# Optimization experiments

Hardware: AMD Instinct MI355X
Metric: run time of the kernel (lower is better)

## Reference

```python
import jax, jax.numpy as jnp
import numpy as np

NEG_SLOPE = 0.2  # PyG GATConv default negative_slope
EPS = 1e-16     # PyG softmax denominator epsilon


def gat_layer(x, src, dst, W, att_src, att_dst, bias, N):
    """PyG-style GATConv: gather -> leaky-relu score -> segment softmax -> scatter-add.
    x: [N, F_in], W: [F_in, H*C], att_src/att_dst: [H, C], bias: [H*C].
    src/dst: [E] edge endpoints (messages flow src -> dst), self-loops included.
    """
    H, C = att_src.shape
    h = (x @ W).reshape(N, H, C)                       # [N, H, C]
    a_s = jnp.sum(h * att_src, axis=-1)                # [N, H]
    a_d = jnp.sum(h * att_dst, axis=-1)                # [N, H]
    e = a_s[src] + a_d[dst]                            # [E, H]
    e = jnp.where(e > 0, e, NEG_SLOPE * e)             # leaky relu
    m = jax.ops.segment_max(e, dst, num_segments=N)    # [N, H] (self-loops ensure every node hit)
    p = jnp.exp(e - m[dst])                            # [E, H]
    s = jax.ops.segment_sum(p, dst, num_segments=N)    # [N, H]
    alpha = p / (s[dst] + EPS)                         # [E, H]
    out = jax.ops.segment_sum(alpha[:, :, None] * h[src], dst, num_segments=N)  # [N, H, C]
    return out.reshape(N, H * C) + bias


def setup_inputs() -> dict:
    key = jax.random.key(0)
    ks = jax.random.split(key, 12)
    N, E = 100000, 1600000
    x = jax.random.normal(ks[0], (N, 1), dtype=jnp.float32)
    edge_index = jax.random.randint(ks[1], (2, E), 0, N, dtype=jnp.int32)
    sc = 0.1
    # conv1: in=1, heads=4, out=8
    W1 = jax.random.normal(ks[2], (1, 32), dtype=jnp.float32) * sc
    att_src1 = jax.random.normal(ks[3], (4, 8), dtype=jnp.float32) * sc
    att_dst1 = jax.random.normal(ks[4], (4, 8), dtype=jnp.float32) * sc
    bias1 = jnp.zeros((32,), dtype=jnp.float32)
    # conv2: in=32, heads=8, out=8
    W2 = jax.random.normal(ks[5], (32, 64), dtype=jnp.float32) * sc
    att_src2 = jax.random.normal(ks[6], (8, 8), dtype=jnp.float32) * sc
    att_dst2 = jax.random.normal(ks[7], (8, 8), dtype=jnp.float32) * sc
    bias2 = jnp.zeros((64,), dtype=jnp.float32)
    # fc2: 64 -> 1
    fc_w = jax.random.normal(ks[8], (64, 1), dtype=jnp.float32) * sc
    fc_b = jnp.zeros((1,), dtype=jnp.float32)
    return {"x": x, "edge_index": edge_index,
            "W1": W1, "att_src1": att_src1, "att_dst1": att_dst1, "bias1": bias1,
            "W2": W2, "att_src2": att_src2, "att_dst2": att_dst2, "bias2": bias2,
            "fc_w": fc_w, "fc_b": fc_b}


def reference(x, edge_index, W1, att_src1, att_dst1, bias1,
              W2, att_src2, att_dst2, bias2, fc_w, fc_b):
    N = x.shape[0]
    loop = jnp.arange(N, dtype=edge_index.dtype)       # add_self_loops=True (PyG default)
    src = jnp.concatenate([edge_index[0], loop])
    dst = jnp.concatenate([edge_index[1], loop])
    h = jax.nn.elu(gat_layer(x, src, dst, W1, att_src1, att_dst1, bias1, N))
    h = jax.nn.elu(gat_layer(h, src, dst, W2, att_src2, att_dst2, bias2, N))
    return h @ fc_w + fc_b                             # [N, 1]
```

## Files before the change

kernel.cpp:

```cpp
#include <hip/hip_runtime.h>
#include <hip/hip_fp16.h>
#include <cmath>

#define TPB 256
#define NSLOPE 0.2f
#define SEPS 1e-16f

#define BSH 7
#define BNODES 128
#define NBMAX 1024
#define NCHUNK 512
#define SCTPB 1024
#define SCSTAGE 3360
#define STAGE 2816
#define MAXDEG 96

__device__ __forceinline__ float lrelu(float v) { return v > 0.f ? v : NSLOPE * v; }
__device__ __forceinline__ float elu1(float v)  { return v > 0.f ? v : expm1f(v); }
__device__ __forceinline__ float elu1f(float v) { return v > 0.f ? v : __expf(v) - 1.f; }

__global__ void k_prep(const float* __restrict__ W1, const float* __restrict__ as1,
                       const float* __restrict__ ad1, float* __restrict__ SD,
                       unsigned* __restrict__ bucketCursor, int NB, unsigned cap) {
    int t = threadIdx.x;
    for (int i = t; i < NB; i += blockDim.x) bucketCursor[(size_t)i * 16] = (unsigned)i * cap;
    if (t < 8) {
        int h = t & 3;
        const float* att = (t >= 4) ? ad1 : as1;
        float acc = 0.f;
        #pragma unroll
        for (int c = 0; c < 8; ++c) acc += W1[h*8+c] * att[h*8+c];
        SD[t] = acc;
    }
}

__global__ void k_bscatter(const int* __restrict__ srcI, const int* __restrict__ dstI,
                           int E, int N, int NB, int chunk,
                           unsigned* __restrict__ bucketCursor, int* __restrict__ pk) {
    __shared__ int cnt[NBMAX];
    __shared__ unsigned base[NBMAX];
    __shared__ int offl[NBMAX];
    __shared__ int rval[SCSTAGE];
    __shared__ unsigned short rbkt[SCSTAGE];
    int t = threadIdx.x;
    int ET = E + N;
    int beg = blockIdx.x * chunk;
    int end = min(beg + chunk, ET);
    int m = end - beg;
    for (int i = t; i < NBMAX; i += blockDim.x) cnt[i] = 0;
    __syncthreads();
    for (int e = beg + t; e < end; e += blockDim.x) {
        int d = (e < E) ? dstI[e] : (e - E);
        atomicAdd(&cnt[d >> BSH], 1);
    }
    __syncthreads();
    int v = (t < NBMAX) ? cnt[t] : 0;
    if (t < NBMAX) base[t] = (unsigned)v;
    __syncthreads();
    for (int off = 1; off < NBMAX; off <<= 1) {
        unsigned u = (t >= off && t < NBMAX) ? base[t - off] : 0u;
        __syncthreads();
        if (t < NBMAX) base[t] += u;
        __syncthreads();
    }
    if (t < NBMAX) offl[t] = (int)base[t] - v;
    __syncthreads();
    if (t < NB) {
        base[t] = v ? atomicAdd(&bucketCursor[(size_t)t * 16], (unsigned)v) : 0u;
        cnt[t] = 0;
    }
    __syncthreads();
    if (m <= SCSTAGE) {
        for (int e = beg + t; e < end; e += blockDim.x) {
            int s, d;
            if (e < E) { s = srcI[e]; d = dstI[e]; } else { s = d = e - E; }
            int b = d >> BSH;
            int r = atomicAdd(&cnt[b], 1);
            int slot = offl[b] + r;
            rval[slot] = (s << BSH) | (d & (BNODES - 1));
            rbkt[slot] = (unsigned short)b;
        }
        __syncthreads();
        for (int slot = t; slot < m; slot += blockDim.x) {
            int b = rbkt[slot];
            pk[base[b] + (unsigned)(slot - offl[b])] = rval[slot];
        }
    } else {
        for (int e = beg + t; e < end; e += blockDim.x) {
            int s, d;
            if (e < E) { s = srcI[e]; d = dstI[e]; } else { s = d = e - E; }
            int b = d >> BSH;
            int r = atomicAdd(&cnt[b], 1);
            pk[base[b] + (unsigned)r] = (s << BSH) | (d & (BNODES - 1));
        }
    }
}

__global__ void k_sl1h2(const int* __restrict__ pk, const unsigned* __restrict__ bucketCursor,
                        unsigned cap,
                        const float* __restrict__ x, const float* __restrict__ SD,
                        const float* __restrict__ W1, const float* __restrict__ b1,
                        const float* __restrict__ W2, const float* __restrict__ attS,
                        const float* __restrict__ attD, int N,
                        unsigned* __restrict__ offsets, int* __restrict__ sortedSrc,
                        __half* __restrict__ h2h, float* __restrict__ aS, float* __restrict__ aD) {
    __shared__ int sorted[STAGE];
    __shared__ int cnt[BNODES];
    __shared__ int offl[BNODES];
    __shared__ float lds1[BNODES][36];
    int b = blockIdx.x, t = threadIdx.x;
    unsigned rbeg = (unsigned)b * cap;
    int m = (int)(bucketCursor[(size_t)b * 16] - rbeg);
    bool inLds = (m <= STAGE);
    int base = b << BSH;
    if (t < BNODES) cnt[t] = 0;
    __syncthreads();
    for (int i = t; i < m; i += TPB) atomicAdd(&cnt[pk[rbeg + i] & (BNODES - 1)], 1);
    __syncthreads();
    int v = (t < BNODES) ? cnt[t] : 0;
    if (t < BNODES) offl[t] = v;
    __syncthreads();
    for (int off = 1; off < BNODES; off <<= 1) {
        int u = (t >= off && t < BNODES) ? offl[t - off] : 0;
        __syncthreads();
        if (t < BNODES) offl[t] += u;
        __syncthreads();
    }
    if (t < BNODES) {
        int ex = offl[t] - v;
        int d = base + t;
        if (d < N) offsets[d] = ((rbeg + (unsigned)ex) << 10) | (unsigned)v;
        cnt[t] = 0;
        offl[t] = ex;
    }
    __syncthreads();
    if (inLds) {
        for (int i = t; i < m; i += TPB) {
            int p = pk[rbeg + i];
            int dl = p & (BNODES - 1);
            int r = atomicAdd(&cnt[dl], 1);
            sorted[offl[dl] + r] = p >> BSH;
        }
        __syncthreads();
        for (int i = t; i < m; i += TPB) sortedSrc[rbeg + i] = sorted[i];
    } else {
        for (int i = t; i < m; i += TPB) {
            int p = pk[rbeg + i];
            int dl = p & (BNODES - 1);
            int r = atomicAdd(&cnt[dl], 1);
            sortedSrc[rbeg + (unsigned)(offl[dl] + r)] = p >> BSH;
        }
        __syncthreads();
    }
    __syncthreads();
    int n = t >> 1, half = t & 1;
    int d2 = base + n;
    bool active = (d2 < N);
    float s0 = 0.f, s1 = 0.f, s2 = 0.f, s3 = 0.f;
    float g0 = 0.f, g1 = 0.f, g2 = 0.f, g3 = 0.f;
    if (active) {
        int deg = cnt[n];
        int lbeg = offl[n];
        float xd = x[d2];
        float S0 = SD[0], S1 = SD[1], S2 = SD[2], S3 = SD[3];
        float D0 = xd*SD[4], D1 = xd*SD[5], D2 = xd*SD[6], D3 = xd*SD[7];
        int dh = (deg + 1) >> 1;
        int i = lbeg + (half ? dh : 0);
        int rem = half ? (deg - dh) : dh;
        for (; rem >= 2; rem -= 2, i += 2) {
            int a0 = inLds ? sorted[i]   : sortedSrc[rbeg + i];
            int a1 = inLds ? sorted[i+1] : sortedSrc[rbeg + i + 1];
            float x0 = x[a0], x1 = x[a1];
            float p;
            p = __expf(lrelu(x0*S0 + D0)); s0 += p; g0 += p * x0;
            p = __expf(lrelu(x0*S1 + D1)); s1 += p; g1 += p * x0;
            p = __expf(lrelu(x0*S2 + D2)); s2 += p; g2 += p * x0;
            p = __expf(lrelu(x0*S3 + D3)); s3 += p; g3 += p * x0;
            p = __expf(lrelu(x1*S0 + D0)); s0 += p; g0 += p * x1;
            p = __expf(lrelu(x1*S1 + D1)); s1 += p; g1 += p * x1;
            p = __expf(lrelu(x1*S2 + D2)); s2 += p; g2 += p * x1;
            p = __expf(lrelu(x1*S3 + D3)); s3 += p; g3 += p * x1;
        }
        if (rem > 0) {
            int a0 = inLds ? sorted[i] : sortedSrc[rbeg + i];
            float xs = x[a0];
            float p;
            p = __expf(lrelu(xs*S0 + D0)); s0 += p; g0 += p * xs;
            p = __expf(lrelu(xs*S1 + D1)); s1 += p; g1 += p * xs;
            p = __expf(lrelu(xs*S2 + D2)); s2 += p; g2 += p * xs;
            p = __expf(lrelu(xs*S3 + D3)); s3 += p; g3 += p * xs;
        }
    }
    s0 += __shfl_xor(s0, 1); s1 += __shfl_xor(s1, 1);
    s2 += __shfl_xor(s2, 1); s3 += __shfl_xor(s3, 1);
    g0 += __shfl_xor(g0, 1); g1 += __shfl_xor(g1, 1);
    g2 += __shfl_xor(g2, 1); g3 += __shfl_xor(g3, 1);
    if (active) {
        float gg[4];
        gg[0] = g0 / (s0 + SEPS); gg[1] = g1 / (s1 + SEPS);
        gg[2] = g2 / (s2 + SEPS); gg[3] = g3 / (s3 + SEPS);
        int h0 = half * 2;
        #pragma unroll
        for (int hh = 0; hh < 2; ++hh)
            #pragma unroll
            for (int cc = 0; cc < 8; ++cc)
                lds1[n][(h0+hh)*8+cc] = elu1(gg[h0+hh] * W1[(h0+hh)*8+cc] + b1[(h0+hh)*8+cc]);
    }
    __syncthreads();
    int lane = t & 63;
    int sub = t >> 6;
    float w2r[32];
    #pragma unroll
    for (int k = 0; k < 32; ++k) w2r[k] = W2[k*64 + lane];
    float attSl = attS[lane], attDl = attD[lane];
    int nCnt = min(BNODES, N - base);
    for (int nn = sub; nn < nCnt; nn += 4) {
        const float4* row4 = (const float4*)lds1[nn];
        float acc = 0.f;
        #pragma unroll
        for (int k4 = 0; k4 < 8; ++k4) {
            float4 rv = row4[k4];
            acc += rv.x*w2r[4*k4] + rv.y*w2r[4*k4+1] + rv.z*w2r[4*k4+2] + rv.w*w2r[4*k4+3];
        }
        int node = base + nn;
        h2h[(size_t)node*64 + lane] = __float2half(acc);
        float ps = acc * attSl;
        float pd = acc * attDl;
        #pragma unroll
        for (int mm = 1; mm < 8; mm <<= 1) {
            ps += __shfl_xor(ps, mm);
            pd += __shfl_xor(pd, mm);
        }
        int hh = lane >> 3, cc = lane & 7;
        if (cc == 0) aS[(size_t)node*8 + hh] = ps;
        if (cc == 1) aD[(size_t)node*8 + hh] = pd;
    }
}

__global__ void k_agg(const unsigned* __restrict__ offsets, const int* __restrict__ ss,
                      const float* __restrict__ aS, const float* __restrict__ aD,
                      const __half* __restrict__ h2h, const float* __restrict__ b2,
                      const float* __restrict__ fcw, const float* __restrict__ fcb,
                      float* __restrict__ out, int N) {
    __shared__ float pl[4][MAXDEG * 8];
    __shared__ int   sl[4][MAXDEG];
    int lane = threadIdx.x & 63;
    int w = threadIdx.x >> 6;
    int d = blockIdx.x * 4 + w;
    if (d >= N) return;
    unsigned u = offsets[d];
    unsigned beg = u >> 10;
    int deg = (int)(u & 1023u);
    int lH   = lane & 31;
    int half = lane >> 5;
    int hh   = lH >> 2;
    float sum = 0.f, ax = 0.f, ay = 0.f;
    if (deg <= MAXDEG) {
        for (int j = lane; j < deg; j += 64) sl[w][j] = ss[beg + j];
        float adp = aD[(size_t)d*8 + (lane & 7)];
        int tot = deg * 8;
        for (int base = 0; base < tot; base += 64) {
            int idx = base + lane;
            if (idx < tot) {
                int s = sl[w][idx >> 3];
                pl[w][idx] = __expf(lrelu(aS[(size_t)s*8 + (lane & 7)] + adp));
            }
        }
        int e = 0;
        for (; e + 8 <= deg; e += 8) {
            int e0 = e + half, e1 = e + 2 + half, e2 = e + 4 + half, e3 = e + 6 + half;
            int s0 = sl[w][e0], s1 = sl[w][e1], s2 = sl[w][e2], s3 = sl[w][e3];
            float p0 = pl[w][e0*8 + hh], p1 = pl[w][e1*8 + hh];
            float p2 = pl[w][e2*8 + hh], p3 = pl[w][e3*8 + hh];
            float2 g0 = __half22float2(*(const __half2*)(h2h + (size_t)s0*64 + 2*lH));
            float2 g1 = __half22float2(*(const __half2*)(h2h + (size_t)s1*64 + 2*lH));
            float2 g2 = __half22float2(*(const __half2*)(h2h + (size_t)s2*64 + 2*lH));
            float2 g3 = __half22float2(*(const __half2*)(h2h + (size_t)s3*64 + 2*lH));
            ax += p0*g0.x + p1*g1.x + p2*g2.x + p3*g3.x;
            ay += p0*g0.y + p1*g1.y + p2*g2.y + p3*g3.y;
            sum += (p0 + p1) + (p2 + p3);
        }
        for (; e + 2 <= deg; e += 2) {
            int e0 = e + half;
            int s0 = sl[w][e0];
            float p0 = pl[w][e0*8 + hh];
            float2 g0 = __half22float2(*(const __half2*)(h2h + (size_t)s0*64 + 2*lH));
            ax += p0*g0.x; ay += p0*g0.y; sum += p0;
        }
        if (e < deg) {
            int s0 = sl[w][e];
            float p0 = (half == 0) ? pl[w][e*8 + hh] : 0.f;
            float2 g0 = __half22float2(*(const __half2*)(h2h + (size_t)s0*64 + 2*lH));
            ax += p0*g0.x; ay += p0*g0.y; sum += p0;
        }
    } else {
        float adh = aD[(size_t)d*8 + hh];
        for (int e = half; e < deg; e += 2) {
            int s = ss[beg + e];
            float p = __expf(lrelu(aS[(size_t)s*8 + hh] + adh));
            float2 g = __half22float2(*(const __half2*)(h2h + (size_t)s*64 + 2*lH));
            ax += p*g.x; ay += p*g.y; sum += p;
        }
    }
    ax  += __shfl_xor(ax, 32);
    ay  += __shfl_xor(ay, 32);
    sum += __shfl_xor(sum, 32);
    float inv = 1.f / (sum + SEPS);
    float tt = elu1f(ax*inv + b2[2*lH]) * fcw[2*lH]
             + elu1f(ay*inv + b2[2*lH+1]) * fcw[2*lH+1];
    #pragma unroll
    for (int m = 16; m; m >>= 1) tt += __shfl_xor(tt, m);
    if (lane == 0) out[d] = tt + fcb[0];
}

extern "C" void kernel_launch(void* const* d_in, const int* in_sizes, int n_in,
                              void* d_out, int out_size, void* d_ws, size_t ws_size,
                              hipStream_t stream) {
    const float* x    = (const float*)d_in[0];
    const int*   ei   = (const int*)  d_in[1];
    const float* W1   = (const float*)d_in[2];
    const float* as1  = (const float*)d_in[3];
    const float* ad1  = (const float*)d_in[4];
    const float* b1   = (const float*)d_in[5];
    const float* W2   = (const float*)d_in[6];
    const float* attS2= (const float*)d_in[7];
    const float* attD2= (const float*)d_in[8];
    const float* b2   = (const float*)d_in[9];
    const float* fcw  = (const float*)d_in[10];
    const float* fcb  = (const float*)d_in[11];
    float* out = (float*)d_out;

    int N = in_sizes[0];
    int E = in_sizes[1] / 2;
    int ET = E + N;
    int NB = (N + BNODES - 1) / BNODES;
    unsigned cap = (unsigned)((ET + NB - 1) / NB + 512);
    cap = (cap + 3u) & ~3u;
    size_t padded = (size_t)NB * cap;

    const int* srcI = ei;
    const int* dstI = ei + E;

    float* ws = (float*)d_ws;
    size_t off = 0;
    float*    SD           = ws + off; off += 16;
    unsigned* bucketCursor = (unsigned*)(ws + off); off += (size_t)NBMAX * 16;
    unsigned* offsets      = (unsigned*)(ws + off); off += (size_t)N + 16;
    int*      pk           = (int*)(ws + off); off += padded;
    int*      sortedSrc    = (int*)(ws + off); off += padded;
    float*    aS2          = ws + off; off += (size_t)N * 8;
    float*    aD2          = ws + off; off += (size_t)N * 8;
    __half*   h2h          = (__half*)(ws + off); off += (size_t)N * 32;

    k_prep<<<1, 1024, 0, stream>>>(W1, as1, ad1, SD, bucketCursor, NB, cap);

    int chunk = (ET + NCHUNK - 1) / NCHUNK;
    k_bscatter<<<NCHUNK, SCTPB, 0, stream>>>(srcI, dstI, E, N, NB, chunk, bucketCursor, pk);
    k_sl1h2   <<<NB, TPB, 0, stream>>>(pk, bucketCursor, cap, x, SD, W1, b1, W2, attS2, attD2,
                                       N, offsets, sortedSrc, h2h, aS2, aD2);
    k_agg     <<<(N + 3) / 4, TPB, 0, stream>>>(offsets, sortedSrc, aS2, aD2, h2h,
                                                b2, fcw, fcb, out, N);
}
```

Measured before the change: 215.5 us.

## Split layer-2 aggregation into two head-group passes over half-width feature tables

The fp16 layer-2 feature table is stored as two separate planes, each holding 4 heads (32 channels) per node. Aggregation then runs in two kernel launches, one per plane, and the second accumulates into the output. Each pass gathers from a table half the size, which is meant to improve cache hit rates for the random source gathers. In exchange the edge list, attention scores and softmax sums are read and computed twice, and there is an extra launch.

```diff
diff --git a/kernel.cpp b/kernel.cpp
--- a/kernel.cpp
+++ b/kernel.cpp
@@ -103,7 +103,7 @@
                         const float* __restrict__ W2, const float* __restrict__ attS,
                         const float* __restrict__ attD, int N,
                         unsigned* __restrict__ offsets, int* __restrict__ sortedSrc,
-                        __half* __restrict__ h2h, float* __restrict__ aS, float* __restrict__ aD) {
+                        __half* __restrict__ h2p, float* __restrict__ aS, float* __restrict__ aD) {
     __shared__ int sorted[STAGE];
     __shared__ int cnt[BNODES];
     __shared__ int offl[BNODES];
@@ -213,6 +213,9 @@
     #pragma unroll
     for (int k = 0; k < 32; ++k) w2r[k] = W2[k*64 + lane];
     float attSl = attS[lane], attDl = attD[lane];
+    size_t N32 = (size_t)N * 32;
+    size_t tabOff = (size_t)(lane >> 5) * N32;
+    int ch = lane & 31;
     int nCnt = min(BNODES, N - base);
     for (int nn = sub; nn < nCnt; nn += 4) {
         const float4* row4 = (const float4*)lds1[nn];
@@ -223,7 +226,7 @@
             acc += rv.x*w2r[4*k4] + rv.y*w2r[4*k4+1] + rv.z*w2r[4*k4+2] + rv.w*w2r[4*k4+3];
         }
         int node = base + nn;
-        h2h[(size_t)node*64 + lane] = __float2half(acc);
+        h2p[tabOff + (size_t)node*32 + ch] = __float2half(acc);
         float ps = acc * attSl;
         float pd = acc * attDl;
         #pragma unroll
@@ -237,12 +240,12 @@
     }
 }
 
-__global__ void k_agg(const unsigned* __restrict__ offsets, const int* __restrict__ ss,
-                      const float* __restrict__ aS, const float* __restrict__ aD,
-                      const __half* __restrict__ h2h, const float* __restrict__ b2,
-                      const float* __restrict__ fcw, const float* __restrict__ fcb,
-                      float* __restrict__ out, int N) {
-    __shared__ float pl[4][MAXDEG * 8];
+__global__ void k_aggp(const unsigned* __restrict__ offsets, const int* __restrict__ ss,
+                       const float* __restrict__ aS, const float* __restrict__ aD,
+                       const __half* __restrict__ h2p, const float* __restrict__ b2,
+                       const float* __restrict__ fcw, const float* __restrict__ fcb,
+                       float* __restrict__ out, int N, int pass) {
+    __shared__ float pl[4][MAXDEG * 4];
     __shared__ int   sl[4][MAXDEG];
     int lane = threadIdx.x & 63;
     int w = threadIdx.x >> 6;
@@ -251,66 +254,64 @@
     unsigned u = offsets[d];
     unsigned beg = u >> 10;
     int deg = (int)(u & 1023u);
-    int lH   = lane & 31;
-    int half = lane >> 5;
-    int hh   = lH >> 2;
+    int eS = lane >> 4;
+    int pr = lane & 15;
+    int hL = pr >> 2;
+    int ho = pass * 4;
+    const __half* tab = h2p + (size_t)pass * ((size_t)N * 32);
     float sum = 0.f, ax = 0.f, ay = 0.f;
     if (deg <= MAXDEG) {
         for (int j = lane; j < deg; j += 64) sl[w][j] = ss[beg + j];
-        float adp = aD[(size_t)d*8 + (lane & 7)];
-        int tot = deg * 8;
+        float adp = aD[(size_t)d*8 + ho + (lane & 3)];
+        int tot = deg * 4;
         for (int base = 0; base < tot; base += 64) {
             int idx = base + lane;
             if (idx < tot) {
-                int s = sl[w][idx >> 3];
-                pl[w][idx] = __expf(lrelu(aS[(size_t)s*8 + (lane & 7)] + adp));
+                int s = sl[w][idx >> 2];
+                pl[w][idx] = __expf(lrelu(aS[(size_t)s*8 + ho + (lane & 3)] + adp));
             }
         }
         int e = 0;
         for (; e + 8 <= deg; e += 8) {
-            int e0 = e + half, e1 = e + 2 + half, e2 = e + 4 + half, e3 = e + 6 + half;
-            int s0 = sl[w][e0], s1 = sl[w][e1], s2 = sl[w][e2], s3 = sl[w][e3];
-            float p0 = pl[w][e0*8 + hh], p1 = pl[w][e1*8 + hh];
-            float p2 = pl[w][e2*8 + hh], p3 = pl[w][e3*8 + hh];
-            float2 g0 = __half22float2(*(const __half2*)(h2h + (size_t)s0*64 + 2*lH));
-            float2 g1 = __half22float2(*(const __half2*)(h2h + (size_t)s1*64 + 2*lH));
-            float2 g2 = __half22float2(*(const __half2*)(h2h + (size_t)s2*64 + 2*lH));
-            float2 g3 = __half22float2(*(const __half2*)(h2h + (size_t)s3*64 + 2*lH));
-            ax += p0*g0.x + p1*g1.x + p2*g2.x + p3*g3.x;
-            ay += p0*g0.y + p1*g1.y + p2*g2.y + p3*g3.y;
-            sum += (p0 + p1) + (p2 + p3);
-        }
-        for (; e + 2 <= deg; e += 2) {
-            int e0 = e + half;
-            int s0 = sl[w][e0];
-            float p0 = pl[w][e0*8 + hh];
-            float2 g0 = __half22float2(*(const __half2*)(h2h + (size_t)s0*64 + 2*lH));
-            ax += p0*g0.x; ay += p0*g0.y; sum += p0;
-        }
-        if (e < deg) {
-            int s0 = sl[w][e];
-            float p0 = (half == 0) ? pl[w][e*8 + hh] : 0.f;
-            float2 g0 = __half22float2(*(const __half2*)(h2h + (size_t)s0*64 + 2*lH));
-            ax += p0*g0.x; ay += p0*g0.y; sum += p0;
+            int ea = e + eS, eb = e + 4 + eS;
+            int sa = sl[w][ea], sb = sl[w][eb];
+            float pa = pl[w][ea*4 + hL], pb = pl[w][eb*4 + hL];
+            float2 ga = __half22float2(*(const __half2*)(tab + (size_t)sa*32 + 2*pr));
+            float2 gb = __half22float2(*(const __half2*)(tab + (size_t)sb*32 + 2*pr));
+            ax += pa*ga.x + pb*gb.x;
+            ay += pa*ga.y + pb*gb.y;
+            sum += pa + pb;
+        }
+        for (; e < deg; e += 4) {
+            int ea = e + eS;
+            bool ok = ea < deg;
+            int sa = sl[w][ok ? ea : 0];
+            float pa = ok ? pl[w][ea*4 + hL] : 0.f;
+            float2 ga = __half22float2(*(const __half2*)(tab + (size_t)sa*32 + 2*pr));
+            ax += pa*ga.x; ay += pa*ga.y; sum += pa;
         }
     } else {
-        float adh = aD[(size_t)d*8 + hh];
-        for (int e = half; e < deg; e += 2) {
+        float adh = aD[(size_t)d*8 + ho + hL];
+        for (int e = eS; e < deg; e += 4) {
             int s = ss[beg + e];
-            float p = __expf(lrelu(aS[(size_t)s*8 + hh] + adh));
-            float2 g = __half22float2(*(const __half2*)(h2h + (size_t)s*64 + 2*lH));
+            float p = __expf(lrelu(aS[(size_t)s*8 + ho + hL] + adh));
+            float2 g = __half22float2(*(const __half2*)(tab + (size_t)s*32 + 2*pr));
             ax += p*g.x; ay += p*g.y; sum += p;
         }
     }
-    ax  += __shfl_xor(ax, 32);
-    ay  += __shfl_xor(ay, 32);
-    sum += __shfl_xor(sum, 32);
+    ax  += __shfl_xor(ax, 16);  ax  += __shfl_xor(ax, 32);
+    ay  += __shfl_xor(ay, 16);  ay  += __shfl_xor(ay, 32);
+    sum += __shfl_xor(sum, 16); sum += __shfl_xor(sum, 32);
     float inv = 1.f / (sum + SEPS);
-    float tt = elu1f(ax*inv + b2[2*lH]) * fcw[2*lH]
-             + elu1f(ay*inv + b2[2*lH+1]) * fcw[2*lH+1];
+    int co = pass * 32 + 2 * pr;
+    float tt = elu1f(ax*inv + b2[co]) * fcw[co]
+             + elu1f(ay*inv + b2[co+1]) * fcw[co+1];
     #pragma unroll
-    for (int m = 16; m; m >>= 1) tt += __shfl_xor(tt, m);
-    if (lane == 0) out[d] = tt + fcb[0];
+    for (int m = 8; m; m >>= 1) tt += __shfl_xor(tt, m);
+    if (lane == 0) {
+        if (pass == 0) out[d] = tt + fcb[0];
+        else           out[d] += tt;
+    }
 }
 
 extern "C" void kernel_launch(void* const* d_in, const int* in_sizes, int n_in,
@@ -350,14 +351,16 @@
     int*      sortedSrc    = (int*)(ws + off); off += padded;
     float*    aS2          = ws + off; off += (size_t)N * 8;
     float*    aD2          = ws + off; off += (size_t)N * 8;
-    __half*   h2h          = (__half*)(ws + off); off += (size_t)N * 32;
+    __half*   h2p          = (__half*)(ws + off); off += (size_t)N * 32;
 
     k_prep<<<1, 1024, 0, stream>>>(W1, as1, ad1, SD, bucketCursor, NB, cap);
 
     int chunk = (ET + NCHUNK - 1) / NCHUNK;
     k_bscatter<<<NCHUNK, SCTPB, 0, stream>>>(srcI, dstI, E, N, NB, chunk, bucketCursor, pk);
     k_sl1h2   <<<NB, TPB, 0, stream>>>(pk, bucketCursor, cap, x, SD, W1, b1, W2, attS2, attD2,
-                                       N, offsets, sortedSrc, h2h, aS2, aD2);
-    k_agg     <<<(N + 3) / 4, TPB, 0, stream>>>(offsets, sortedSrc, aS2, aD2, h2h,
-                                                b2, fcw, fcb, out, N);
-}
+                                       N, offsets, sortedSrc, h2p, aS2, aD2);
+    k_aggp    <<<(N + 3) / 4, TPB, 0, stream>>>(offsets, sortedSrc, aS2, aD2, h2p,
+                                                b2, fcw, fcb, out, N, 0);
+    k_aggp    <<<(N + 3) / 4, TPB, 0, stream>>>(offsets, sortedSrc, aS2, aD2, h2p,
+                                                b2, fcw, fcb, out, N, 1);
+}
```

Measured after the change: 264.6 us. 1.23x slower.
